# Performance work log

Measured on AMD Instinct MI355X. Metric: run time of the kernel, lower is better.

The kernel has to match this reference:

```python
import jax, jax.numpy as jnp
import numpy as np

B, H, L = 8, 256, 8192

def setup_inputs() -> dict:
    key = jax.random.key(0)
    k1, k2, k3 = jax.random.split(key, 3)
    u = jax.random.normal(k1, (B, H, L), dtype=jnp.float32)
    K = jax.random.normal(k2, (H, L), dtype=jnp.float32)
    # D ~ uniform_ring with min=max=1.0, field='real' -> random signs on unit ring
    D = jnp.where(jax.random.uniform(k3, (H,)) < 0.5, -1.0, 1.0).astype(jnp.float32)
    return {"u": u, "K": K, "D": D}

def reference(u, K, D):
    # FFT-based circular long convolution per channel: y = ifft(fft(u) * fft(K)).real
    u_s = jnp.fft.fft(u, axis=-1)            # (B,H,L) complex
    k_s = jnp.fft.fft(K, axis=-1)            # (H,L)   complex
    y = jnp.fft.ifft(u_s * k_s[None], axis=-1).real  # (B,H,L)
    y = y + D[None, :, None] * u             # skip connection D*u
    y = jnp.tanh(y)
    return y
```

## Files before the change

kernel.cpp:

```cpp
#include <hip/hip_runtime.h>
#include <math.h>


#define LL 8192
#define NT 256
#define HH 256
#define TWO_PI 6.2831853071795864f
#define CP16 0.980785280403230f
#define SP16 0.195090322016128f
#define CP8  0.92387953251129f
#define SP8  0.38268343236509f

__device__ __forceinline__ int SW(int e) {
    return e ^ ((e >> 4) & 15) ^ (((e >> 8) & 1) << 4);
}
__device__ __forceinline__ float fast_tanh(float x) {
    float e = __expf(2.0f * x);
    return 1.0f - 2.0f / (e + 1.0f);
}

template<int JT>
__device__ __forceinline__ void fill_pyr_cs(float c0, float s0, float Er, float Ei,
                                            float* twr, float* twi) {
    const int off = (1 << JT) - 1;
    twr[off] = c0; twi[off] = s0;
    #pragma unroll
    for (int m = 1; m < (1 << JT); ++m) {
        const float pr = twr[off + m - 1], pi = twi[off + m - 1];
        twr[off + m] = pr * Er - pi * Ei;
        twi[off + m] = pr * Ei + pi * Er;
    }
    #pragma unroll
    for (int j = JT - 1; j >= 0; --j) {
        #pragma unroll
        for (int m = 0; m < (1 << j); ++m) {
            const float a = twr[(2 << j) - 1 + m], b = twi[(2 << j) - 1 + m];
            twr[(1 << j) - 1 + m] = a * a - b * b;
            twi[(1 << j) - 1 + m] = 2.0f * a * b;
        }
    }
}
template<int JT>
__device__ __forceinline__ void fill_pyr(float ang0, float Er, float Ei,
                                         float* twr, float* twi) {
    float s, c;
    __sincosf(ang0, &s, &c);
    fill_pyr_cs<JT>(c, s, Er, Ei, twr, twi);
}

template<int R2>
__device__ __forceinline__ void dif_apply(float* xr, float* xi,
                                          const float* twr, const float* twi) {
    #pragma unroll
    for (int j = R2 - 1; j >= 0; --j) {
        #pragma unroll
        for (int q = 0; q < (1 << (R2 - 1)); ++q) {
            const int mm = q & ((1 << j) - 1);
            const int m0 = ((q >> j) << (j + 1)) | mm;
            const int m1 = m0 + (1 << j);
            const float wr = twr[(1 << j) - 1 + mm], wi = twi[(1 << j) - 1 + mm];
            const float ar = xr[m0], ai = xi[m0], br = xr[m1], bi = xi[m1];
            xr[m0] = ar + br; xi[m0] = ai + bi;
            const float dr = ar - br, di = ai - bi;
            xr[m1] = dr * wr - di * wi;
            xi[m1] = dr * wi + di * wr;
        }
    }
}
template<int R2>
__device__ __forceinline__ void dit_apply(float* xr, float* xi,
                                          const float* twr, const float* twi) {
    #pragma unroll
    for (int j = 0; j < R2; ++j) {
        #pragma unroll
        for (int q = 0; q < (1 << (R2 - 1)); ++q) {
            const int mm = q & ((1 << j) - 1);
            const int m0 = ((q >> j) << (j + 1)) | mm;
            const int m1 = m0 + (1 << j);
            const float wr = twr[(1 << j) - 1 + mm], wi = twi[(1 << j) - 1 + mm];
            const float br = xr[m1] * wr - xi[m1] * wi;
            const float bi = xr[m1] * wi + xi[m1] * wr;
            const float ar = xr[m0], ai = xi[m0];
            xr[m0] = ar + br; xi[m0] = ai + bi;
            xr[m1] = ar - br; xi[m1] = ai - bi;
        }
    }
}

__device__ __forceinline__ void fwd_A(float* xr, float* xi, int tid,
                                      float* re, float* im) {
    float twr[31], twi[31];
    fill_pyr<4>(-(TWO_PI / 8192.0f) * (float)tid, CP16, -SP16, twr, twi);
    dif_apply<5>(xr, xi, twr, twi);
    #pragma unroll
    for (int m = 0; m < 32; ++m) {
        const int p = SW(tid + (m << 8));
        re[p] = xr[m]; im[p] = xi[m];
    }
}

__global__ __launch_bounds__(NT) void kfft_kernel(const float* __restrict__ K,
                                                  const float* __restrict__ D,
                                                  float2* __restrict__ Kf) {
    __shared__ float re[LL];
    __shared__ float im[LL];
    const int h = blockIdx.x;
    const int tid = threadIdx.x;
    const float* Kr = K + (size_t)h * LL;
    float xr[32], xi[32];
    #pragma unroll
    for (int m = 0; m < 32; ++m) {
        xr[m] = Kr[tid + (m << 8)];
        xi[m] = 0.0f;
    }
    fwd_A(xr, xi, tid, re, im);
    __syncthreads();

    const int lane = tid & 63, wv = tid >> 6;
    const int q = lane & 15, qw = (lane >> 4) & 3;

    {
        float twr[15], twi[15];
        fill_pyr<3>(-(TWO_PI / 256.0f) * (float)q, CP8, -SP8, twr, twi);
        #pragma unroll
        for (int r = 0; r < 2; ++r) {
            const int c = (wv << 3) + qw + (r << 2);
            const int base = (c << 8) + q;
            float ar[16], ai[16];
            #pragma unroll
            for (int m = 0; m < 16; ++m) {
                const int p = SW(base + (m << 4));
                ar[m] = re[p]; ai[m] = im[p];
            }
            dif_apply<4>(ar, ai, twr, twi);
            #pragma unroll
            for (int m = 0; m < 16; ++m) {
                const int p = SW(base + (m << 4));
                re[p] = ar[m]; im[p] = ai[m];
            }
        }
    }
    {
        const float dh = D[h];
        const float invN = 1.0f / (float)LL;
        float twr[15], twi[15];
        fill_pyr_cs<3>(1.0f, 0.0f, CP8, -SP8, twr, twi);
        #pragma unroll
        for (int r = 0; r < 2; ++r) {
            const int c = (wv << 3) + qw + (r << 2);
            const int eb = (c << 8) + (q << 4);
            float yr[16], yi[16];
            #pragma unroll
            for (int j = 0; j < 16; ++j) {
                const int p = SW(eb + j);
                yr[j] = re[p]; yi[j] = im[p];
            }
            dif_apply<4>(yr, yi, twr, twi);
            float4* o4 = (float4*)(Kf + (size_t)h * LL + eb);
            #pragma unroll
            for (int jj = 0; jj < 8; ++jj) {
                float4 v;
                v.x = (yr[2 * jj]     + dh) * invN; v.y = yi[2 * jj]     * invN;
                v.z = (yr[2 * jj + 1] + dh) * invN; v.w = yi[2 * jj + 1] * invN;
                o4[jj] = v;
            }
        }
    }
}

__global__ __launch_bounds__(NT) void conv_kernel(const float* __restrict__ u,
                                                  const float2* __restrict__ Kf,
                                                  float* __restrict__ out) {
    __shared__ float re[LL];
    __shared__ float im[LL];
    const int tid = threadIdx.x;
    const int h = blockIdx.x & (HH - 1);
    const int pr_ = blockIdx.x >> 8;
    const size_t off0 = ((size_t)(pr_ * 2) * HH + h) * LL;
    const size_t off1 = off0 + (size_t)HH * LL;
    const float* u0 = u + off0;
    const float* u1 = u + off1;

    float xr[32], xi[32];
    #pragma unroll
    for (int m = 0; m < 32; ++m) {
        xr[m] = u0[tid + (m << 8)];
        xi[m] = u1[tid + (m << 8)];
    }
    fwd_A(xr, xi, tid, re, im);
    __syncthreads();

    const int lane = tid & 63, wv = tid >> 6;
    const int q = lane & 15, qw = (lane >> 4) & 3;
    const int c0 = (wv << 3) + qw;
    const float2* kf = Kf + (size_t)h * LL;

    float kwr[2][16], kwi[2][16];
    #pragma unroll
    for (int r = 0; r < 2; ++r) {
        const int eb = ((c0 + (r << 2)) << 8) + (q << 4);
        const float4* kp = (const float4*)(kf + eb);
        #pragma unroll
        for (int jj = 0; jj < 8; ++jj) {
            const float4 v = kp[jj];
            kwr[r][2 * jj] = v.x;     kwi[r][2 * jj] = v.y;
            kwr[r][2 * jj + 1] = v.z; kwi[r][2 * jj + 1] = v.w;
        }
    }

    {
        float twr[15], twi[15];
        fill_pyr<3>(-(TWO_PI / 256.0f) * (float)q, CP8, -SP8, twr, twi);
        #pragma unroll
        for (int r = 0; r < 2; ++r) {
            const int base = ((c0 + (r << 2)) << 8) + q;
            float ar[16], ai[16];
            #pragma unroll
            for (int m = 0; m < 16; ++m) {
                const int p = SW(base + (m << 4));
                ar[m] = re[p]; ai[m] = im[p];
            }
            dif_apply<4>(ar, ai, twr, twi);
            #pragma unroll
            for (int m = 0; m < 16; ++m) {
                const int p = SW(base + (m << 4));
                re[p] = ar[m]; im[p] = ai[m];
            }
        }
    }
    {
        float twd_r[15], twd_i[15], twu_r[15], twu_i[15];
        fill_pyr_cs<3>(1.0f, 0.0f, CP8, -SP8, twd_r, twd_i);
        fill_pyr_cs<3>(1.0f, 0.0f, CP8, SP8, twu_r, twu_i);
        #pragma unroll
        for (int r = 0; r < 2; ++r) {
            const int eb = ((c0 + (r << 2)) << 8) + (q << 4);
            float yr[16], yi[16];
            #pragma unroll
            for (int j = 0; j < 16; ++j) {
                const int p = SW(eb + j);
                yr[j] = re[p]; yi[j] = im[p];
            }
            dif_apply<4>(yr, yi, twd_r, twd_i);
            #pragma unroll
            for (int j = 0; j < 16; ++j) {
                const float a = yr[j], b = yi[j];
                yr[j] = a * kwr[r][j] - b * kwi[r][j];
                yi[j] = a * kwi[r][j] + b * kwr[r][j];
            }
            dit_apply<4>(yr, yi, twu_r, twu_i);
            #pragma unroll
            for (int j = 0; j < 16; ++j) {
                const int p = SW(eb + j);
                re[p] = yr[j]; im[p] = yi[j];
            }
        }
    }
    {
        float twr[15], twi[15];
        fill_pyr<3>((TWO_PI / 256.0f) * (float)q, CP8, SP8, twr, twi);
        #pragma unroll
        for (int r = 0; r < 2; ++r) {
            const int base = ((c0 + (r << 2)) << 8) + q;
            float ar[16], ai[16];
            #pragma unroll
            for (int m = 0; m < 16; ++m) {
                const int p = SW(base + (m << 4));
                ar[m] = re[p]; ai[m] = im[p];
            }
            dit_apply<4>(ar, ai, twr, twi);
            #pragma unroll
            for (int m = 0; m < 16; ++m) {
                const int p = SW(base + (m << 4));
                re[p] = ar[m]; im[p] = ai[m];
            }
        }
    }
    __syncthreads();

    {
        float twr[31], twi[31];
        #pragma unroll
        for (int m = 0; m < 32; ++m) {
            const int p = SW(tid + (m << 8));
            xr[m] = re[p]; xi[m] = im[p];
        }
        fill_pyr<4>((TWO_PI / 8192.0f) * (float)tid, CP16, SP16, twr, twi);
        dit_apply<5>(xr, xi, twr, twi);
    }
    float* o0 = out + off0;
    float* o1 = out + off1;
    #pragma unroll
    for (int m = 0; m < 32; ++m) {
        const int n = tid + (m << 8);
        o0[n] = fast_tanh(xr[m]);
        o1[n] = fast_tanh(xi[m]);
    }
}

extern "C" void kernel_launch(void* const* d_in, const int* in_sizes, int n_in,
                              void* d_out, int out_size, void* d_ws, size_t ws_size,
                              hipStream_t stream) {
    const float* u = (const float*)d_in[0];
    const float* K = (const float*)d_in[1];
    const float* D = (const float*)d_in[2];
    float* out = (float*)d_out;
    float2* Kf = (float2*)d_ws;

    kfft_kernel<<<dim3(HH), dim3(NT), 0, stream>>>(K, D, Kf);
    conv_kernel<<<dim3(4 * HH), dim3(NT), 0, stream>>>(u, Kf, out);
}
```

Measured before the change: 156.4 us.

## Restructure FFT to 512 threads with radix-16 outer and radix-8 inner passes

```diff
diff --git a/kernel.cpp b/kernel.cpp
--- a/kernel.cpp
+++ b/kernel.cpp
@@ -3,16 +3,16 @@
 
 
 #define LL 8192
-#define NT 256
+#define NT 512
 #define HH 256
 #define TWO_PI 6.2831853071795864f
-#define CP16 0.980785280403230f
-#define SP16 0.195090322016128f
 #define CP8  0.92387953251129f
 #define SP8  0.38268343236509f
+#define CP4  0.70710678118654752f
+#define SP4  0.70710678118654752f
 
 __device__ __forceinline__ int SW(int e) {
-    return e ^ ((e >> 4) & 15) ^ (((e >> 8) & 1) << 4);
+    return e ^ ((e >> 3) & 0x18) ^ ((e >> 6) & 7);
 }
 __device__ __forceinline__ float fast_tanh(float x) {
     float e = __expf(2.0f * x);
@@ -89,76 +89,104 @@
 
 __device__ __forceinline__ void fwd_A(float* xr, float* xi, int tid,
                                       float* re, float* im) {
-    float twr[31], twi[31];
-    fill_pyr<4>(-(TWO_PI / 8192.0f) * (float)tid, CP16, -SP16, twr, twi);
-    dif_apply<5>(xr, xi, twr, twi);
-    #pragma unroll
-    for (int m = 0; m < 32; ++m) {
-        const int p = SW(tid + (m << 8));
+    float twr[15], twi[15];
+    fill_pyr<3>(-(TWO_PI / 8192.0f) * (float)tid, CP8, -SP8, twr, twi);
+    dif_apply<4>(xr, xi, twr, twi);
+    #pragma unroll
+    for (int m = 0; m < 16; ++m) {
+        const int p = SW(tid + (m << 9));
         re[p] = xr[m]; im[p] = xi[m];
     }
 }
 
-__global__ __launch_bounds__(NT) void kfft_kernel(const float* __restrict__ K,
-                                                  const float* __restrict__ D,
-                                                  float2* __restrict__ Kf) {
+template<bool INV>
+__device__ __forceinline__ void mid_M1(float* re, float* im, int lane, int wv) {
+    float twr[7], twi[7];
+    const float sgn = INV ? 1.0f : -1.0f;
+    fill_pyr<2>(sgn * (TWO_PI / 512.0f) * (float)lane, CP4, sgn * SP4, twr, twi);
+    #pragma unroll
+    for (int r = 0; r < 2; ++r) {
+        const int base = (((wv << 1) | r) << 9) + lane;
+        float ar[8], ai[8];
+        #pragma unroll
+        for (int j = 0; j < 8; ++j) {
+            const int p = SW(base + (j << 6));
+            ar[j] = re[p]; ai[j] = im[p];
+        }
+        if (INV) dit_apply<3>(ar, ai, twr, twi);
+        else     dif_apply<3>(ar, ai, twr, twi);
+        #pragma unroll
+        for (int j = 0; j < 8; ++j) {
+            const int p = SW(base + (j << 6));
+            re[p] = ar[j]; im[p] = ai[j];
+        }
+    }
+}
+
+template<bool INV>
+__device__ __forceinline__ void mid_M2(float* re, float* im, int lane, int wv) {
+    float twr[7], twi[7];
+    const float sgn = INV ? 1.0f : -1.0f;
+    fill_pyr<2>(sgn * (TWO_PI / 64.0f) * (float)(lane & 7), CP4, sgn * SP4, twr, twi);
+    const int sub = ((lane >> 3) << 6) + (lane & 7);
+    #pragma unroll
+    for (int r = 0; r < 2; ++r) {
+        const int base = (((wv << 1) | r) << 9) + sub;
+        float ar[8], ai[8];
+        #pragma unroll
+        for (int j = 0; j < 8; ++j) {
+            const int p = SW(base + (j << 3));
+            ar[j] = re[p]; ai[j] = im[p];
+        }
+        if (INV) dit_apply<3>(ar, ai, twr, twi);
+        else     dif_apply<3>(ar, ai, twr, twi);
+        #pragma unroll
+        for (int j = 0; j < 8; ++j) {
+            const int p = SW(base + (j << 3));
+            re[p] = ar[j]; im[p] = ai[j];
+        }
+    }
+}
+
+__global__ __launch_bounds__(NT, 4) void kfft_kernel(const float* __restrict__ K,
+                                                     const float* __restrict__ D,
+                                                     float2* __restrict__ Kf) {
     __shared__ float re[LL];
     __shared__ float im[LL];
     const int h = blockIdx.x;
     const int tid = threadIdx.x;
     const float* Kr = K + (size_t)h * LL;
-    float xr[32], xi[32];
-    #pragma unroll
-    for (int m = 0; m < 32; ++m) {
-        xr[m] = Kr[tid + (m << 8)];
+    float xr[16], xi[16];
+    #pragma unroll
+    for (int m = 0; m < 16; ++m) {
+        xr[m] = Kr[tid + (m << 9)];
         xi[m] = 0.0f;
     }
     fwd_A(xr, xi, tid, re, im);
     __syncthreads();
 
     const int lane = tid & 63, wv = tid >> 6;
-    const int q = lane & 15, qw = (lane >> 4) & 3;
-
-    {
-        float twr[15], twi[15];
-        fill_pyr<3>(-(TWO_PI / 256.0f) * (float)q, CP8, -SP8, twr, twi);
-        #pragma unroll
-        for (int r = 0; r < 2; ++r) {
-            const int c = (wv << 3) + qw + (r << 2);
-            const int base = (c << 8) + q;
-            float ar[16], ai[16];
-            #pragma unroll
-            for (int m = 0; m < 16; ++m) {
-                const int p = SW(base + (m << 4));
-                ar[m] = re[p]; ai[m] = im[p];
-            }
-            dif_apply<4>(ar, ai, twr, twi);
-            #pragma unroll
-            for (int m = 0; m < 16; ++m) {
-                const int p = SW(base + (m << 4));
-                re[p] = ar[m]; im[p] = ai[m];
-            }
-        }
-    }
+    mid_M1<false>(re, im, lane, wv);
+    mid_M2<false>(re, im, lane, wv);
+
     {
         const float dh = D[h];
         const float invN = 1.0f / (float)LL;
-        float twr[15], twi[15];
-        fill_pyr_cs<3>(1.0f, 0.0f, CP8, -SP8, twr, twi);
+        float twd_r[7], twd_i[7];
+        fill_pyr_cs<2>(1.0f, 0.0f, CP4, -SP4, twd_r, twd_i);
         #pragma unroll
         for (int r = 0; r < 2; ++r) {
-            const int c = (wv << 3) + qw + (r << 2);
-            const int eb = (c << 8) + (q << 4);
-            float yr[16], yi[16];
-            #pragma unroll
-            for (int j = 0; j < 16; ++j) {
+            const int eb = (((wv << 1) | r) << 9) + (lane << 3);
+            float yr[8], yi[8];
+            #pragma unroll
+            for (int j = 0; j < 8; ++j) {
                 const int p = SW(eb + j);
                 yr[j] = re[p]; yi[j] = im[p];
             }
-            dif_apply<4>(yr, yi, twr, twi);
+            dif_apply<3>(yr, yi, twd_r, twd_i);
             float4* o4 = (float4*)(Kf + (size_t)h * LL + eb);
             #pragma unroll
-            for (int jj = 0; jj < 8; ++jj) {
+            for (int jj = 0; jj < 4; ++jj) {
                 float4 v;
                 v.x = (yr[2 * jj]     + dh) * invN; v.y = yi[2 * jj]     * invN;
                 v.z = (yr[2 * jj + 1] + dh) * invN; v.w = yi[2 * jj + 1] * invN;
@@ -168,9 +196,9 @@
     }
 }
 
-__global__ __launch_bounds__(NT) void conv_kernel(const float* __restrict__ u,
-                                                  const float2* __restrict__ Kf,
-                                                  float* __restrict__ out) {
+__global__ __launch_bounds__(NT, 4) void conv_kernel(const float* __restrict__ u,
+                                                     const float2* __restrict__ Kf,
+                                                     float* __restrict__ out) {
     __shared__ float re[LL];
     __shared__ float im[LL];
     const int tid = threadIdx.x;
@@ -181,118 +209,82 @@
     const float* u0 = u + off0;
     const float* u1 = u + off1;
 
-    float xr[32], xi[32];
-    #pragma unroll
-    for (int m = 0; m < 32; ++m) {
-        xr[m] = u0[tid + (m << 8)];
-        xi[m] = u1[tid + (m << 8)];
+    float xr[16], xi[16];
+    #pragma unroll
+    for (int m = 0; m < 16; ++m) {
+        xr[m] = u0[tid + (m << 9)];
+        xi[m] = u1[tid + (m << 9)];
     }
     fwd_A(xr, xi, tid, re, im);
     __syncthreads();
 
     const int lane = tid & 63, wv = tid >> 6;
-    const int q = lane & 15, qw = (lane >> 4) & 3;
-    const int c0 = (wv << 3) + qw;
     const float2* kf = Kf + (size_t)h * LL;
 
-    float kwr[2][16], kwi[2][16];
+    float kwr[2][8], kwi[2][8];
     #pragma unroll
     for (int r = 0; r < 2; ++r) {
-        const int eb = ((c0 + (r << 2)) << 8) + (q << 4);
+        const int eb = (((wv << 1) | r) << 9) + (lane << 3);
         const float4* kp = (const float4*)(kf + eb);
         #pragma unroll
-        for (int jj = 0; jj < 8; ++jj) {
+        for (int jj = 0; jj < 4; ++jj) {
             const float4 v = kp[jj];
             kwr[r][2 * jj] = v.x;     kwi[r][2 * jj] = v.y;
             kwr[r][2 * jj + 1] = v.z; kwi[r][2 * jj + 1] = v.w;
         }
     }
 
+    mid_M1<false>(re, im, lane, wv);
+    mid_M2<false>(re, im, lane, wv);
+
     {
-        float twr[15], twi[15];
-        fill_pyr<3>(-(TWO_PI / 256.0f) * (float)q, CP8, -SP8, twr, twi);
+        float twd_r[7], twd_i[7], twu_r[7], twu_i[7];
+        fill_pyr_cs<2>(1.0f, 0.0f, CP4, -SP4, twd_r, twd_i);
+        fill_pyr_cs<2>(1.0f, 0.0f, CP4, SP4, twu_r, twu_i);
         #pragma unroll
         for (int r = 0; r < 2; ++r) {
-            const int base = ((c0 + (r << 2)) << 8) + q;
-            float ar[16], ai[16];
-            #pragma unroll
-            for (int m = 0; m < 16; ++m) {
-                const int p = SW(base + (m << 4));
-                ar[m] = re[p]; ai[m] = im[p];
-            }
-            dif_apply<4>(ar, ai, twr, twi);
-            #pragma unroll
-            for (int m = 0; m < 16; ++m) {
-                const int p = SW(base + (m << 4));
-                re[p] = ar[m]; im[p] = ai[m];
-            }
-        }
-    }
-    {
-        float twd_r[15], twd_i[15], twu_r[15], twu_i[15];
-        fill_pyr_cs<3>(1.0f, 0.0f, CP8, -SP8, twd_r, twd_i);
-        fill_pyr_cs<3>(1.0f, 0.0f, CP8, SP8, twu_r, twu_i);
-        #pragma unroll
-        for (int r = 0; r < 2; ++r) {
-            const int eb = ((c0 + (r << 2)) << 8) + (q << 4);
-            float yr[16], yi[16];
-            #pragma unroll
-            for (int j = 0; j < 16; ++j) {
+            const int eb = (((wv << 1) | r) << 9) + (lane << 3);
+            float yr[8], yi[8];
+            #pragma unroll
+            for (int j = 0; j < 8; ++j) {
                 const int p = SW(eb + j);
                 yr[j] = re[p]; yi[j] = im[p];
             }
-            dif_apply<4>(yr, yi, twd_r, twd_i);
-            #pragma unroll
-            for (int j = 0; j < 16; ++j) {
+            dif_apply<3>(yr, yi, twd_r, twd_i);
+            #pragma unroll
+            for (int j = 0; j < 8; ++j) {
                 const float a = yr[j], b = yi[j];
                 yr[j] = a * kwr[r][j] - b * kwi[r][j];
                 yi[j] = a * kwi[r][j] + b * kwr[r][j];
             }
-            dit_apply<4>(yr, yi, twu_r, twu_i);
-            #pragma unroll
-            for (int j = 0; j < 16; ++j) {
+            dit_apply<3>(yr, yi, twu_r, twu_i);
+            #pragma unroll
+            for (int j = 0; j < 8; ++j) {
                 const int p = SW(eb + j);
                 re[p] = yr[j]; im[p] = yi[j];
             }
         }
     }
+
+    mid_M2<true>(re, im, lane, wv);
+    mid_M1<true>(re, im, lane, wv);
+    __syncthreads();
+
     {
         float twr[15], twi[15];
-        fill_pyr<3>((TWO_PI / 256.0f) * (float)q, CP8, SP8, twr, twi);
-        #pragma unroll
-        for (int r = 0; r < 2; ++r) {
-            const int base = ((c0 + (r << 2)) << 8) + q;
-            float ar[16], ai[16];
-            #pragma unroll
-            for (int m = 0; m < 16; ++m) {
-                const int p = SW(base + (m << 4));
-                ar[m] = re[p]; ai[m] = im[p];
-            }
-            dit_apply<4>(ar, ai, twr, twi);
-            #pragma unroll
-            for (int m = 0; m < 16; ++m) {
-                const int p = SW(base + (m << 4));
-                re[p] = ar[m]; im[p] = ai[m];
-            }
-        }
-    }
-    __syncthreads();
-
-    {
-        float twr[31], twi[31];
-        #pragma unroll
-        for (int m = 0; m < 32; ++m) {
-            const int p = SW(tid + (m << 8));
+        #pragma unroll
+        for (int m = 0; m < 16; ++m) {
+            const int p = SW(tid + (m << 9));
             xr[m] = re[p]; xi[m] = im[p];
         }
-        fill_pyr<4>((TWO_PI / 8192.0f) * (float)tid, CP16, SP16, twr, twi);
-        dit_apply<5>(xr, xi, twr, twi);
+        fill_pyr<3>((TWO_PI / 8192.0f) * (float)tid, CP8, SP8, twr, twi);
+        dit_apply<4>(xr, xi, twr, twi);
     }
     float* o0 = out + off0;
     float* o1 = out + off1;
     #pragma unroll
-    for (int m = 0; m < 32; ++m) {
-        const int n = tid + (m << 8);
+    for (int m = 0; m < 16; ++m) {
+        const int n = tid + (m << 9);
         o0[n] = fast_tanh(xr[m]);
         o1[n] = fast_tanh(xi[m]);
     }
```

New measurement: 150.5 us. 1.04x faster.
